# Optimization experiments

Measured on AMD Instinct MI355X. Metric: run time of the kernel, lower is better.

The kernel has to match this reference:

```python
import jax, jax.numpy as jnp
import numpy as np

NY, NX, DIM = 4096, 50000, 3
RADIUS = 1.4
BOX = 14.3  # chosen so ~16 y-neighbors per x point at radius 1.4
LAYERS = [3, 128, 256, 3]  # kernel_in_dim=3 -> hidden [128,256] -> dim=3


def _radius_neighbors(x, y, r):
    """Brute-force radius search: edges (x_index i, nbr_index j) with |x_i - y_j| <= r."""
    r2 = r * r
    xi, yj = [], []
    for s in range(0, x.shape[0], 5000):
        xc = x[s:s + 5000]
        d2 = ((xc[:, None, :] - y[None, :, :]) ** 2).sum(-1)
        ii, jj = np.nonzero(d2 <= r2)
        xi.append(ii + s)
        yj.append(jj)
    return np.concatenate(yj).astype(np.int64), np.concatenate(xi).astype(np.int64)


def setup_inputs() -> dict:
    rng = np.random.default_rng(0)
    y = rng.uniform(0.0, BOX, (NY, DIM)).astype(np.float32)   # rom_ic points
    x = rng.uniform(0.0, BOX, (NX, DIM)).astype(np.float32)   # fom_ic points
    f_y = rng.standard_normal((NY, DIM)).astype(np.float32)   # rom_f values
    nbr_index, x_index = _radius_neighbors(x, y, RADIUS)

    key = jax.random.key(0)
    ks = jax.random.split(key, 3)
    params = {}
    for i in range(3):
        fan_in = LAYERS[i]
        params[f"W{i+1}"] = (jax.random.normal(ks[i], (LAYERS[i], LAYERS[i + 1]), jnp.float32)
                             / np.float32(np.sqrt(fan_in)))
        params[f"b{i+1}"] = jnp.zeros((LAYERS[i + 1],), jnp.float32)

    return dict(rom_ic=jnp.asarray(y)[None], fom_ic=jnp.asarray(x)[None],
                rom_f=jnp.asarray(f_y)[None],
                nbr_index=jnp.asarray(nbr_index), x_index=jnp.asarray(x_index),
                **params)


def _kernel_mlp(h, W1, b1, W2, b2, W3, b3):
    h = jax.nn.gelu(h @ W1 + b1)
    h = jax.nn.gelu(h @ W2 + b2)
    return h @ W3 + b3


def reference(rom_ic, fom_ic, rom_f, W1, b1, W2, b2, W3, b3, nbr_index, x_index):
    y = rom_ic[0]      # [NY,3] source points
    x = fom_ic[0]      # [NX,3] target points
    f_y = rom_f[0]     # [NY,3] source function values

    rel = y[nbr_index] - x[x_index]                    # [E,3] per-edge kernel input
    k = _kernel_mlp(rel, W1, b1, W2, b2, W3, b3)       # [E,3] kernel values
    msg = k * f_y[nbr_index]                           # 'linear' transform: k(x,y) * f(y)

    num = jax.ops.segment_sum(msg, x_index, num_segments=x.shape[0])        # [NX,3]
    cnt = jax.ops.segment_sum(jnp.ones((msg.shape[0],), msg.dtype), x_index,
                              num_segments=x.shape[0])                      # [NX]
    out = num / jnp.maximum(cnt, 1.0)[:, None]         # mean over neighbors (0 if none)
    return out[None]                                    # [1, NX, 3]
```

## Files before the change

### kernel.cpp

```cpp
#include <hip/hip_runtime.h>
#include <hip/hip_bf16.h>

typedef __bf16 bf16x8 __attribute__((ext_vector_type(8)));
typedef float  f32x4  __attribute__((ext_vector_type(4)));
typedef float  f32x2  __attribute__((ext_vector_type(2)));
typedef float  f32x16 __attribute__((ext_vector_type(16)));
typedef int    i32x4  __attribute__((ext_vector_type(4)));

__device__ __forceinline__ f32x2 gelu2(f32x2 x) {
    f32x2 x2 = x * x;
    f32x2 t  = x2 * 0.044715f + 1.0f;
    f32x2 a  = (x * -1.5957691216057308f) * t;
    f32x2 e  = { __expf(a.x), __expf(a.y) };
    f32x2 d  = e + 1.0f;
    f32x2 r  = { __builtin_amdgcn_rcpf(d.x), __builtin_amdgcn_rcpf(d.y) };
    return x * r;
}

__device__ __forceinline__ unsigned int pack2bf(float a, float b) {
    unsigned short ua = __builtin_bit_cast(unsigned short, (__bf16)a);
    unsigned short ub = __builtin_bit_cast(unsigned short, (__bf16)b);
    return (unsigned int)ua | ((unsigned int)ub << 16);
}

__device__ __forceinline__ bf16x8 frag_from_pk(unsigned int q0, unsigned int q1,
                                               unsigned int q2, unsigned int q3) {
    auto p02 = __builtin_amdgcn_permlane32_swap((int)q0, (int)q2, false, false);
    auto p13 = __builtin_amdgcn_permlane32_swap((int)q1, (int)q3, false, false);
    i32x4 fri = { static_cast<int>(p02[0]), static_cast<int>(p13[0]),
                  static_cast<int>(p02[1]), static_cast<int>(p13[1]) };
    return __builtin_bit_cast(bf16x8, fri);
}

__global__ void prep_weights(const float* __restrict__ W2, const float* __restrict__ W3,
                             const float* __restrict__ W1,
                             __bf16* __restrict__ w2t, __bf16* __restrict__ w3t,
                             __bf16* __restrict__ w1tp) {
    int idx = blockIdx.x * 256 + threadIdx.x;
    if (idx < 32768) {
        int k = idx >> 8;
        int u = idx & 255;
        w2t[u * 128 + k] = (__bf16)W2[idx];
    } else if (idx < 32768 + 8192) {
        int t = idx - 32768;
        int d = t >> 8;
        int u = t & 255;
        w3t[t] = (__bf16)(d < 3 ? W3[u * 3 + d] : 0.0f);
    } else if (idx < 32768 + 8192 + 2048) {
        int t = idx - 40960;
        int u = t >> 4;
        int k = t & 15;
        w1tp[t] = (k < 3) ? (__bf16)W1[k * 128 + u] : (__bf16)0.0f;
    }
}

__launch_bounds__(512, 4)
__global__ void edge_mlp(const float* __restrict__ y, const float* __restrict__ x,
                         const float* __restrict__ fy,
                         const int* __restrict__ nbr, const int* __restrict__ xidx,
                         const __bf16* __restrict__ w1tp, const float* __restrict__ b1,
                         const __bf16* __restrict__ w2t, const float* __restrict__ b2,
                         const __bf16* __restrict__ w3t, const float* __restrict__ b3,
                         float* __restrict__ out, int E) {
    __shared__ __attribute__((aligned(16))) __bf16 w2l[256 * 128];
    __shared__ __attribute__((aligned(16))) __bf16 relT[8][32][16];
    __shared__ float msgS[8][32][3];
    __shared__ int   isS[8][32];

    const int tid  = threadIdx.x;
    const int wid  = tid >> 6;
    const int lane = tid & 63;
    const int l31  = lane & 31;
    const int b    = lane >> 5;

    {
        int u = tid >> 1, half = tid & 1;
        const __bf16* src = w2t + u * 128 + half * 64;
        char* rowbase = (char*)w2l + u * 256;
        int sw = (u & 15) << 4;
        #pragma unroll
        for (int j = 0; j < 8; ++j) {
            bf16x8 v = *(const bf16x8*)(src + j * 8);
            int colb = half * 128 + j * 16;
            *(bf16x8*)(rowbase + (colb ^ sw)) = v;
        }
    }

    const int g = blockIdx.x * 256 + wid * 32 + l31;
    int   iidx = -1;
    float fy0 = 0.0f, fy1 = 0.0f, fy2 = 0.0f;
    if (b == 0) {
        bf16x8 rv = { (__bf16)0.0f, (__bf16)0.0f, (__bf16)0.0f, (__bf16)0.0f,
                      (__bf16)0.0f, (__bf16)0.0f, (__bf16)0.0f, (__bf16)0.0f };
        if (g < E) {
            int j = nbr[g];
            iidx  = xidx[g];
            rv[0] = (__bf16)(y[j*3+0] - x[iidx*3+0]);
            rv[1] = (__bf16)(y[j*3+1] - x[iidx*3+1]);
            rv[2] = (__bf16)(y[j*3+2] - x[iidx*3+2]);
            fy0 = fy[j*3+0];
            fy1 = fy[j*3+1];
            fy2 = fy[j*3+2];
        }
        *(bf16x8*)&relT[wid][l31][0] = rv;
        *(bf16x8*)&relT[wid][l31][8] = (bf16x8){ (__bf16)0.0f, (__bf16)0.0f, (__bf16)0.0f, (__bf16)0.0f,
                                                 (__bf16)0.0f, (__bf16)0.0f, (__bf16)0.0f, (__bf16)0.0f };
    }
    __syncthreads();

    bf16x8 relB = *(const bf16x8*)&relT[wid][l31][b * 8];
    bf16x8 B2[8];

    #pragma unroll
    for (int ut1 = 0; ut1 < 4; ++ut1) {
        f32x16 c;
        #pragma unroll
        for (int q = 0; q < 16; ++q) c[q] = 0.0f;
        bf16x8 a1 = *(const bf16x8*)&w1tp[(ut1 * 32 + l31) * 16 + b * 8];
        c = __builtin_amdgcn_mfma_f32_32x32x16_bf16(a1, relB, c, 0, 0, 0);

        int u0 = ut1 * 32 + 4 * b;
        f32x4 b1q[4];
        #pragma unroll
        for (int gq = 0; gq < 4; ++gq)
            b1q[gq] = *(const f32x4*)(b1 + u0 + 8 * gq);

        unsigned int pw[8];
        #pragma unroll
        for (int gq = 0; gq < 4; ++gq) {
            f32x2 s01 = { c[4*gq+0] + b1q[gq][0], c[4*gq+1] + b1q[gq][1] };
            f32x2 s23 = { c[4*gq+2] + b1q[gq][2], c[4*gq+3] + b1q[gq][3] };
            f32x2 g01 = gelu2(s01);
            f32x2 g23 = gelu2(s23);
            pw[2*gq+0] = pack2bf(g01.x, g01.y);
            pw[2*gq+1] = pack2bf(g23.x, g23.y);
        }
        B2[2*ut1+0] = frag_from_pk(pw[0], pw[1], pw[2], pw[3]);
        B2[2*ut1+1] = frag_from_pk(pw[4], pw[5], pw[6], pw[7]);
    }

    f32x16 acc3;
    #pragma unroll
    for (int q = 0; q < 16; ++q) acc3[q] = 0.0f;

    #pragma unroll
    for (int ut = 0; ut < 8; ++ut) {
        f32x16 c;
        #pragma unroll
        for (int q = 0; q < 16; ++q) c[q] = 0.0f;
        {
            const int u = ut * 32 + l31;
            const char* rowbase = (const char*)w2l + u * 256;
            const int sw = (u & 15) << 4;
            #pragma unroll
            for (int kt = 0; kt < 8; ++kt) {
                bf16x8 a2 = *(const bf16x8*)(rowbase + ((kt * 32 + b * 16) ^ sw));
                c = __builtin_amdgcn_mfma_f32_32x32x16_bf16(a2, B2[kt], c, 0, 0, 0);
            }
        }

        int u0 = ut * 32 + 4 * b;
        f32x4 b2q[4];
        #pragma unroll
        for (int gq = 0; gq < 4; ++gq)
            b2q[gq] = *(const f32x4*)(b2 + u0 + 8 * gq);

        unsigned int pw[8];
        #pragma unroll
        for (int gq = 0; gq < 4; ++gq) {
            f32x2 s01 = { c[4*gq+0] + b2q[gq][0], c[4*gq+1] + b2q[gq][1] };
            f32x2 s23 = { c[4*gq+2] + b2q[gq][2], c[4*gq+3] + b2q[gq][3] };
            f32x2 g01 = gelu2(s01);
            f32x2 g23 = gelu2(s23);
            pw[2*gq+0] = pack2bf(g01.x, g01.y);
            pw[2*gq+1] = pack2bf(g23.x, g23.y);
        }

        #pragma unroll
        for (int ki = 0; ki < 2; ++ki) {
            bf16x8 bfr = frag_from_pk(pw[4*ki+0], pw[4*ki+1], pw[4*ki+2], pw[4*ki+3]);
            bf16x8 a3  = *(const bf16x8*)&w3t[l31 * 256 + ut * 32 + ki * 16 + b * 8];
            acc3 = __builtin_amdgcn_mfma_f32_32x32x16_bf16(a3, bfr, acc3, 0, 0, 0);
        }
    }

    if (b == 0) {
        float m0 = 0.0f, m1 = 0.0f, m2 = 0.0f;
        if (iidx >= 0) {
            m0 = (acc3[0] + b3[0]) * fy0;
            m1 = (acc3[1] + b3[1]) * fy1;
            m2 = (acc3[2] + b3[2]) * fy2;
        }
        msgS[wid][l31][0] = m0;
        msgS[wid][l31][1] = m1;
        msgS[wid][l31][2] = m2;
        isS[wid][l31] = iidx;
        bool leader = (iidx >= 0) && (l31 == 0 || isS[wid][l31 - 1] != iidx);
        if (leader) {
            float s0 = 0.0f, s1 = 0.0f, s2 = 0.0f;
            int j = l31;
            while (j < 32 && isS[wid][j] == iidx) {
                s0 += msgS[wid][j][0];
                s1 += msgS[wid][j][1];
                s2 += msgS[wid][j][2];
                ++j;
            }
            unsafeAtomicAdd(&out[iidx*3+0], s0);
            unsafeAtomicAdd(&out[iidx*3+1], s1);
            unsafeAtomicAdd(&out[iidx*3+2], s2);
        }
    }
}

__global__ void finalize_div(float* __restrict__ out, const int* __restrict__ xidx,
                             int E, int nx) {
    int i = blockIdx.x * blockDim.x + threadIdx.x;
    if (i >= nx) return;
    int lo = 0, hi = E;
    while (lo < hi) { int mid = (lo + hi) >> 1; if (xidx[mid] < i) lo = mid + 1; else hi = mid; }
    int start = lo;
    hi = E;
    while (lo < hi) { int mid = (lo + hi) >> 1; if (xidx[mid] < i + 1) lo = mid + 1; else hi = mid; }
    int cnt = lo - start;
    float inv = 1.0f / (float)(cnt > 1 ? cnt : 1);
    out[i*3+0] *= inv;
    out[i*3+1] *= inv;
    out[i*3+2] *= inv;
}

extern "C" void kernel_launch(void* const* d_in, const int* in_sizes, int n_in,
                              void* d_out, int out_size, void* d_ws, size_t ws_size,
                              hipStream_t stream) {
    const float* y   = (const float*)d_in[0];
    const float* x   = (const float*)d_in[1];
    const float* fyp = (const float*)d_in[2];
    const int*   nbr = (const int*)d_in[3];
    const int*   xix = (const int*)d_in[4];
    const float* W1  = (const float*)d_in[5];
    const float* b1  = (const float*)d_in[6];
    const float* W2  = (const float*)d_in[7];
    const float* b2  = (const float*)d_in[8];
    const float* W3  = (const float*)d_in[9];
    const float* b3  = (const float*)d_in[10];
    float* out = (float*)d_out;

    int E  = in_sizes[3];
    int nx = in_sizes[1] / 3;
    __bf16* w2t  = (__bf16*)d_ws;
    __bf16* w3t  = (__bf16*)((char*)d_ws + 65536);
    __bf16* w1tp = (__bf16*)((char*)d_ws + 81920);

    hipMemsetAsync(d_out, 0, (size_t)out_size * sizeof(float), stream);
    prep_weights<<<168, 256, 0, stream>>>(W2, W3, W1, w2t, w3t, w1tp);

    int nblocks = (E + 255) / 256;
    edge_mlp<<<nblocks, 512, 0, stream>>>(y, x, fyp, nbr, xix, w1tp, b1, w2t, b2, w3t, b3, out, E);

    finalize_div<<<(nx + 255) / 256, 256, 0, stream>>>(out, xix, E, nx);
}
```

Before: 142.9 us.

## Halve W2 LDS footprint by staging in two phases and raise occupancy

Only half of W2 (128 rows) is kept in LDS at a time, so the layer-2 loop runs in two phases with a barrier-guarded reload between them. This cuts LDS per block from about 80KB to about 40KB, and the launch-bounds hint rises from 4 to 8 blocks per CU to allow more concurrent blocks. The relT LDS staging for edge inputs is removed; the bf16 fragment is now built directly in registers, with the upper lanes zero. In exchange there are extra __syncthreads and a mid-kernel global reload of W2 per block, and the tighter register budget may cause spills.

```diff
diff --git a/kernel.cpp b/kernel.cpp
--- a/kernel.cpp
+++ b/kernel.cpp
@@ -54,7 +54,7 @@
     }
 }
 
-__launch_bounds__(512, 4)
+__launch_bounds__(512, 8)
 __global__ void edge_mlp(const float* __restrict__ y, const float* __restrict__ x,
                          const float* __restrict__ fy,
                          const int* __restrict__ nbr, const int* __restrict__ xidx,
@@ -62,8 +62,7 @@
                          const __bf16* __restrict__ w2t, const float* __restrict__ b2,
                          const __bf16* __restrict__ w3t, const float* __restrict__ b3,
                          float* __restrict__ out, int E) {
-    __shared__ __attribute__((aligned(16))) __bf16 w2l[256 * 128];
-    __shared__ __attribute__((aligned(16))) __bf16 relT[8][32][16];
+    __shared__ __attribute__((aligned(16))) __bf16 w2l[128 * 128];
     __shared__ float msgS[8][32][3];
     __shared__ int   isS[8][32];
 
@@ -73,44 +72,36 @@
     const int l31  = lane & 31;
     const int b    = lane >> 5;
 
-    {
-        int u = tid >> 1, half = tid & 1;
-        const __bf16* src = w2t + u * 128 + half * 64;
-        char* rowbase = (char*)w2l + u * 256;
-        int sw = (u & 15) << 4;
-        #pragma unroll
-        for (int j = 0; j < 8; ++j) {
-            bf16x8 v = *(const bf16x8*)(src + j * 8);
-            int colb = half * 128 + j * 16;
-            *(bf16x8*)(rowbase + (colb ^ sw)) = v;
-        }
-    }
-
     const int g = blockIdx.x * 256 + wid * 32 + l31;
     int   iidx = -1;
     float fy0 = 0.0f, fy1 = 0.0f, fy2 = 0.0f;
-    if (b == 0) {
-        bf16x8 rv = { (__bf16)0.0f, (__bf16)0.0f, (__bf16)0.0f, (__bf16)0.0f,
-                      (__bf16)0.0f, (__bf16)0.0f, (__bf16)0.0f, (__bf16)0.0f };
-        if (g < E) {
-            int j = nbr[g];
-            iidx  = xidx[g];
-            rv[0] = (__bf16)(y[j*3+0] - x[iidx*3+0]);
-            rv[1] = (__bf16)(y[j*3+1] - x[iidx*3+1]);
-            rv[2] = (__bf16)(y[j*3+2] - x[iidx*3+2]);
-            fy0 = fy[j*3+0];
-            fy1 = fy[j*3+1];
-            fy2 = fy[j*3+2];
-        }
-        *(bf16x8*)&relT[wid][l31][0] = rv;
-        *(bf16x8*)&relT[wid][l31][8] = (bf16x8){ (__bf16)0.0f, (__bf16)0.0f, (__bf16)0.0f, (__bf16)0.0f,
-                                                 (__bf16)0.0f, (__bf16)0.0f, (__bf16)0.0f, (__bf16)0.0f };
-    }
-    __syncthreads();
-
-    bf16x8 relB = *(const bf16x8*)&relT[wid][l31][b * 8];
+    bf16x8 rv = { (__bf16)0.0f, (__bf16)0.0f, (__bf16)0.0f, (__bf16)0.0f,
+                  (__bf16)0.0f, (__bf16)0.0f, (__bf16)0.0f, (__bf16)0.0f };
+    if (b == 0 && g < E) {
+        int j = nbr[g];
+        iidx  = xidx[g];
+        rv[0] = (__bf16)(y[j*3+0] - x[iidx*3+0]);
+        rv[1] = (__bf16)(y[j*3+1] - x[iidx*3+1]);
+        rv[2] = (__bf16)(y[j*3+2] - x[iidx*3+2]);
+        fy0 = fy[j*3+0];
+        fy1 = fy[j*3+1];
+        fy2 = fy[j*3+2];
+    }
+    const bf16x8 relB = rv;
+
+    {
+        int ul = tid >> 2, q = tid & 3;
+        const __bf16* src = w2t + ul * 128 + q * 32;
+        char* rowbase = (char*)w2l + ul * 256;
+        int sw = (ul & 15) << 4;
+        #pragma unroll
+        for (int j = 0; j < 4; ++j) {
+            bf16x8 v = *(const bf16x8*)(src + j * 8);
+            *(bf16x8*)(rowbase + ((q * 64 + j * 16) ^ sw)) = v;
+        }
+    }
+
     bf16x8 B2[8];
-
     #pragma unroll
     for (int ut1 = 0; ut1 < 4; ++ut1) {
         f32x16 c;
@@ -138,49 +129,68 @@
         B2[2*ut1+0] = frag_from_pk(pw[0], pw[1], pw[2], pw[3]);
         B2[2*ut1+1] = frag_from_pk(pw[4], pw[5], pw[6], pw[7]);
     }
+    __syncthreads();
 
     f32x16 acc3;
     #pragma unroll
     for (int q = 0; q < 16; ++q) acc3[q] = 0.0f;
 
     #pragma unroll
-    for (int ut = 0; ut < 8; ++ut) {
-        f32x16 c;
-        #pragma unroll
-        for (int q = 0; q < 16; ++q) c[q] = 0.0f;
-        {
-            const int u = ut * 32 + l31;
-            const char* rowbase = (const char*)w2l + u * 256;
-            const int sw = (u & 15) << 4;
-            #pragma unroll
-            for (int kt = 0; kt < 8; ++kt) {
-                bf16x8 a2 = *(const bf16x8*)(rowbase + ((kt * 32 + b * 16) ^ sw));
-                c = __builtin_amdgcn_mfma_f32_32x32x16_bf16(a2, B2[kt], c, 0, 0, 0);
-            }
-        }
-
-        int u0 = ut * 32 + 4 * b;
-        f32x4 b2q[4];
-        #pragma unroll
-        for (int gq = 0; gq < 4; ++gq)
-            b2q[gq] = *(const f32x4*)(b2 + u0 + 8 * gq);
-
-        unsigned int pw[8];
-        #pragma unroll
-        for (int gq = 0; gq < 4; ++gq) {
-            f32x2 s01 = { c[4*gq+0] + b2q[gq][0], c[4*gq+1] + b2q[gq][1] };
-            f32x2 s23 = { c[4*gq+2] + b2q[gq][2], c[4*gq+3] + b2q[gq][3] };
-            f32x2 g01 = gelu2(s01);
-            f32x2 g23 = gelu2(s23);
-            pw[2*gq+0] = pack2bf(g01.x, g01.y);
-            pw[2*gq+1] = pack2bf(g23.x, g23.y);
-        }
-
-        #pragma unroll
-        for (int ki = 0; ki < 2; ++ki) {
-            bf16x8 bfr = frag_from_pk(pw[4*ki+0], pw[4*ki+1], pw[4*ki+2], pw[4*ki+3]);
-            bf16x8 a3  = *(const bf16x8*)&w3t[l31 * 256 + ut * 32 + ki * 16 + b * 8];
-            acc3 = __builtin_amdgcn_mfma_f32_32x32x16_bf16(a3, bfr, acc3, 0, 0, 0);
+    for (int phase = 0; phase < 2; ++phase) {
+        if (phase == 1) {
+            __syncthreads();
+            int ul = tid >> 2, q = tid & 3;
+            const __bf16* src = w2t + (128 + ul) * 128 + q * 32;
+            char* rowbase = (char*)w2l + ul * 256;
+            int sw = (ul & 15) << 4;
+            #pragma unroll
+            for (int j = 0; j < 4; ++j) {
+                bf16x8 v = *(const bf16x8*)(src + j * 8);
+                *(bf16x8*)(rowbase + ((q * 64 + j * 16) ^ sw)) = v;
+            }
+            __syncthreads();
+        }
+
+        #pragma unroll
+        for (int utl = 0; utl < 4; ++utl) {
+            f32x16 c;
+            #pragma unroll
+            for (int q = 0; q < 16; ++q) c[q] = 0.0f;
+            {
+                const int ul = utl * 32 + l31;
+                const char* rowbase = (const char*)w2l + ul * 256;
+                const int sw = (ul & 15) << 4;
+                #pragma unroll
+                for (int kt = 0; kt < 8; ++kt) {
+                    bf16x8 a2 = *(const bf16x8*)(rowbase + ((kt * 32 + b * 16) ^ sw));
+                    c = __builtin_amdgcn_mfma_f32_32x32x16_bf16(a2, B2[kt], c, 0, 0, 0);
+                }
+            }
+
+            const int ubase = phase * 128 + utl * 32;
+            int u0 = ubase + 4 * b;
+            f32x4 b2q[4];
+            #pragma unroll
+            for (int gq = 0; gq < 4; ++gq)
+                b2q[gq] = *(const f32x4*)(b2 + u0 + 8 * gq);
+
+            unsigned int pw[8];
+            #pragma unroll
+            for (int gq = 0; gq < 4; ++gq) {
+                f32x2 s01 = { c[4*gq+0] + b2q[gq][0], c[4*gq+1] + b2q[gq][1] };
+                f32x2 s23 = { c[4*gq+2] + b2q[gq][2], c[4*gq+3] + b2q[gq][3] };
+                f32x2 g01 = gelu2(s01);
+                f32x2 g23 = gelu2(s23);
+                pw[2*gq+0] = pack2bf(g01.x, g01.y);
+                pw[2*gq+1] = pack2bf(g23.x, g23.y);
+            }
+
+            #pragma unroll
+            for (int ki = 0; ki < 2; ++ki) {
+                bf16x8 bfr = frag_from_pk(pw[4*ki+0], pw[4*ki+1], pw[4*ki+2], pw[4*ki+3]);
+                bf16x8 a3  = *(const bf16x8*)&w3t[l31 * 256 + ubase + ki * 16 + b * 8];
+                acc3 = __builtin_amdgcn_mfma_f32_32x32x16_bf16(a3, bfr, acc3, 0, 0, 0);
+            }
         }
     }
 
```

New measurement: 545.3 us. +281.7%, slower.
